# Kernel tuning notes

Measured on AMD Instinct MI355X. Metric: run time of the kernel, lower is better.

## Reference

```python
import jax, jax.numpy as jnp
import numpy as np
from jax import lax

B, N = 16, 2048
S0, S1, K = 256, 128, 32
EPS = 1e-5


def bn_relu(x, gamma, beta, axes):
    # training-mode BatchNorm (batch statistics) + ReLU; channel is last dim
    mean = jnp.mean(x, axis=axes, keepdims=True)
    var = jnp.var(x, axis=axes, keepdims=True)
    return jax.nn.relu((x - mean) * lax.rsqrt(var + EPS) * gamma + beta)


def fps(coords, s):
    # farthest point sampling, deterministic start at index 0. coords [B,N,3]
    b, n, _ = coords.shape
    def body(carry, _):
        dist, far = carry
        centroid = jnp.take_along_axis(coords, far[:, None, None], axis=1)  # [B,1,3]
        d = jnp.sum((coords - centroid) ** 2, axis=-1)                      # [B,N]
        dist = jnp.minimum(dist, d)
        return (dist, jnp.argmax(dist, axis=-1).astype(jnp.int32)), far
    init = (jnp.full((b, n), 1e10, coords.dtype), jnp.zeros((b,), jnp.int32))
    _, idx = lax.scan(body, init, None, length=s)
    return jnp.transpose(idx)  # [B,s]


def gather_points(pts, idx):
    # pts [B,N,C], idx [B,...] int -> [B,...,C]
    flat = idx.reshape(idx.shape[0], -1)[..., None]  # [B,M,1]
    out = jnp.take_along_axis(pts, flat, axis=1)     # [B,M,C]
    return out.reshape(*idx.shape, pts.shape[-1])


def sample_and_knn_group(s, k, coords, features):
    # coords [B,N,3], features [B,N,C] -> new_xyz [B,s,3], agg [B,s,k,2C]
    fps_idx = fps(coords, s)
    new_xyz = gather_points(coords, fps_idx)      # [B,s,3]
    center = gather_points(features, fps_idx)     # [B,s,C]
    d2 = jnp.sum((new_xyz[:, :, None, :] - coords[:, None, :, :]) ** 2, axis=-1)  # [B,s,N]
    _, knn_idx = lax.top_k(-d2, k)                # k smallest distances
    grouped = gather_points(features, knn_idx)    # [B,s,k,C]
    agg = jnp.concatenate(
        [grouped - center[:, :, None, :],
         jnp.broadcast_to(center[:, :, None, :], grouped.shape)], axis=-1)
    return new_xyz, agg


def sg_block(coords, features, s, k, w, gamma, beta):
    # conv1x1 -> BN -> ReLU -> max over k neighbors
    new_xyz, nf = sample_and_knn_group(s, k, coords, features)  # nf [B,s,k,d]
    h = jnp.einsum('bskd,od->bsko', nf, w)
    h = bn_relu(h, gamma, beta, axes=(0, 1, 2))
    return new_xyz, jnp.max(h, axis=2)  # [B,s,out]


def setup_inputs() -> dict:
    key = jax.random.key(0)
    ks = jax.random.split(key, 5)
    return {
        'x': jax.random.normal(ks[0], (B, 3, N), jnp.float32),
        'w1': jax.random.normal(ks[1], (64, 3), jnp.float32) * (1.0 / np.sqrt(3)),
        'g1': jnp.ones((64,), jnp.float32), 'b1': jnp.zeros((64,), jnp.float32),
        'w2': jax.random.normal(ks[2], (64, 64), jnp.float32) * 0.125,
        'g2': jnp.ones((64,), jnp.float32), 'b2': jnp.zeros((64,), jnp.float32),
        'w_sg0': jax.random.normal(ks[3], (128, 128), jnp.float32) * (1.0 / np.sqrt(128)),
        'g_sg0': jnp.ones((128,), jnp.float32), 'b_sg0': jnp.zeros((128,), jnp.float32),
        'w_sg1': jax.random.normal(ks[4], (256, 256), jnp.float32) * (1.0 / np.sqrt(256)),
        'g_sg1': jnp.ones((256,), jnp.float32), 'b_sg1': jnp.zeros((256,), jnp.float32),
    }


def reference(x, w1, g1, b1, w2, g2, b2, w_sg0, g_sg0, b_sg0, w_sg1, g_sg1, b_sg1):
    coords = jnp.transpose(x, (0, 2, 1))                   # [B,N,3]
    f = bn_relu(jnp.einsum('bnc,oc->bno', coords, w1), g1, b1, axes=(0, 1))  # [B,N,64]
    f = bn_relu(jnp.einsum('bnc,oc->bno', f, w2), g2, b2, axes=(0, 1))       # [B,N,64]
    xyz1, f1 = sg_block(coords, f, S0, K, w_sg0, g_sg0, b_sg0)   # [B,S0,128]
    _, f2 = sg_block(xyz1, f1, S1, K, w_sg1, g_sg1, b_sg1)       # [B,S1,256]
    return jnp.transpose(f2, (0, 2, 1))                           # [B,256,S1]
```

## Files before the change

### kernel.cpp

```cpp
#include <hip/hip_runtime.h>
#include <float.h>

#define BATCH 16
#define NPTS  2048
#define NS0   256
#define NS1   128
#define KK    32
#define EPSV  1e-5f
#define MROWS 32768.0f
#define M0F   131072.0f
#define M1F   65536.0f

__device__ __forceinline__ float sqdist(float ax,float ay,float az,float bx,float by,float bz){
  float dx=__fsub_rn(ax,bx), dy=__fsub_rn(ay,by), dz=__fsub_rn(az,bz);
  return __fadd_rn(__fadd_rn(__fmul_rn(dx,dx),__fmul_rn(dy,dy)),__fmul_rn(dz,dz));
}

template<int CTRL,int RM>
__device__ __forceinline__ float dpp_fmax_s(float x){
  int t = __builtin_amdgcn_update_dpp((int)0xFF800000, __float_as_int(x), CTRL, RM, 0xf, false);
  return fmaxf(x, __int_as_float(t));
}
template<int CTRL,int RM>
__device__ __forceinline__ float dpp_fmin_s(float x){
  int t = __builtin_amdgcn_update_dpp(0x7F800000, __float_as_int(x), CTRL, RM, 0xf, false);
  return fminf(x, __int_as_float(t));
}
template<int CTRL,int RM>
__device__ __forceinline__ unsigned dpp_umin_s(unsigned x){
  unsigned t = (unsigned)__builtin_amdgcn_update_dpp(-1, (int)x, CTRL, RM, 0xf, false);
  return t<x ? t : x;
}
__device__ __forceinline__ void wave_argmax_f32(float v, unsigned idx, float& mall, int& sel){
  float m=v;
  m=dpp_fmax_s<0x111,0xf>(m); m=dpp_fmax_s<0x112,0xf>(m); m=dpp_fmax_s<0x114,0xf>(m);
  m=dpp_fmax_s<0x118,0xf>(m); m=dpp_fmax_s<0x142,0xa>(m); m=dpp_fmax_s<0x143,0xc>(m);
  mall = __int_as_float(__builtin_amdgcn_readlane(__float_as_int(m),63));
  unsigned c = (v==mall)? idx : 0xFFFFFFFFu;
  c=dpp_umin_s<0x111,0xf>(c); c=dpp_umin_s<0x112,0xf>(c); c=dpp_umin_s<0x114,0xf>(c);
  c=dpp_umin_s<0x118,0xf>(c); c=dpp_umin_s<0x142,0xa>(c); c=dpp_umin_s<0x143,0xc>(c);
  sel = (int)(unsigned)__builtin_amdgcn_readlane((int)c,63);
}
__device__ __forceinline__ int wave_argmin_f32(float v, unsigned idx){
  float m=v;
  m=dpp_fmin_s<0x111,0xf>(m); m=dpp_fmin_s<0x112,0xf>(m); m=dpp_fmin_s<0x114,0xf>(m);
  m=dpp_fmin_s<0x118,0xf>(m); m=dpp_fmin_s<0x142,0xa>(m); m=dpp_fmin_s<0x143,0xc>(m);
  float mall = __int_as_float(__builtin_amdgcn_readlane(__float_as_int(m),63));
  unsigned c = (v==mall)? idx : 0xFFFFFFFFu;
  c=dpp_umin_s<0x111,0xf>(c); c=dpp_umin_s<0x112,0xf>(c); c=dpp_umin_s<0x114,0xf>(c);
  c=dpp_umin_s<0x118,0xf>(c); c=dpp_umin_s<0x142,0xa>(c); c=dpp_umin_s<0x143,0xc>(c);
  return (int)(unsigned)__builtin_amdgcn_readlane((int)c,63);
}


__device__ void embed1_body(int bid, const float* __restrict__ x, const float* __restrict__ w1,
                            float* __restrict__ coords, float* __restrict__ t1){
  __shared__ float w[192];
  __shared__ float xs[3][64];
  __shared__ float fin[64][65];
  int tid = threadIdx.x;
  if (tid < 192) w[tid] = w1[tid];
  int base = bid*64;
  int b = base / NPTS, n0 = base % NPTS;
  if (tid < 192){
    int ch = tid>>6, i = tid&63;
    xs[ch][i] = x[((size_t)b*3+ch)*NPTS + n0 + i];
  }
  __syncthreads();
  if (tid < 64){
    coords[(size_t)(base+tid)*3+0]=xs[0][tid];
    coords[(size_t)(base+tid)*3+1]=xs[1][tid];
    coords[(size_t)(base+tid)*3+2]=xs[2][tid];
  }
  int p = tid>>2, c0 = (tid&3)<<4;
  float cx=xs[0][p], cy=xs[1][p], cz=xs[2][p];
  #pragma unroll
  for(int j=0;j<16;j++){
    int c = c0+j;
    fin[p][c] = cx*w[c*3+0] + cy*w[c*3+1] + cz*w[c*3+2];
  }
  __syncthreads();
  for(int i=tid;i<4096;i+=256){
    int pp=i>>6, c=i&63;
    t1[(size_t)base*64 + i] = fin[pp][c];
  }
}

__device__ void wt_body(int gid, const float* __restrict__ w0, float* __restrict__ wt0,
                        const float* __restrict__ w1, float* __restrict__ wt1){
  if(gid < 128*128){
    int o = gid % 128, c = gid / 128;
    wt0[gid] = w0[o*128 + c];
  } else {
    int g2 = gid - 128*128;
    if(g2 >= 256*256) return;
    int o = g2 % 256, c = g2 / 256;
    wt1[g2] = w1[o*256 + c];
  }
}

__device__ void statsA_body(int blk, const float* __restrict__ t,
                            float* __restrict__ accS, float* __restrict__ accQ){
  int c = threadIdx.x;
  int r0 = blk*128;
  float s=0.f, q=0.f;
  for(int r=0;r<128;r++){
    float v = t[(size_t)(r0+r)*64 + c];
    s+=v; q+=v*v;
  }
  atomicAdd(accS+c, s);
  atomicAdd(accQ+c, q);
}

__device__ void embed2_body(int bid, const float* __restrict__ t1, const float* __restrict__ w2,
                            const float* __restrict__ accS, const float* __restrict__ accQ,
                            const float* __restrict__ g1, const float* __restrict__ b1,
                            float* __restrict__ t2,
                            float* __restrict__ acc2S, float* __restrict__ acc2Q,
                            float* ls, float* lq, char* smem){
  float (*fin)[64] = (float(*)[64])smem;
  float* sm = (float*)smem + 4096;
  float* sr = sm+64; float* sg = sr+64; float* sb = sg+64;
  int tid = threadIdx.x;
  if (tid<64){
    float S=accS[tid], Q=accQ[tid];
    float m = S/MROWS, v = Q/MROWS - m*m; if(v<0.f) v=0.f;
    sm[tid]=m; sr[tid]=rsqrtf(v+EPSV); sg[tid]=g1[tid]; sb[tid]=b1[tid];
    ls[tid]=0.f; lq[tid]=0.f;
  }
  __syncthreads();
  int base = bid*64;
  for(int i=tid;i<4096;i+=256){
    int p=i>>6, c=i&63;
    float v = t1[(size_t)(base+p)*64 + c];
    v = (v - sm[c])*sr[c]*sg[c] + sb[c];
    fin[p][c] = v>0.f ? v : 0.f;
  }
  __syncthreads();
  int o = tid & 63, p0 = tid>>6;
  float acc[16];
  #pragma unroll
  for(int i=0;i<16;i++) acc[i]=0.f;
  for(int cc=0; cc<64; cc+=4){
    float4 wv = *(const float4*)(w2 + o*64 + cc);
    #pragma unroll
    for(int i=0;i<16;i++){
      float4 f4 = *(const float4*)&fin[p0 + i*4][cc];
      acc[i] += f4.x*wv.x + f4.y*wv.y + f4.z*wv.z + f4.w*wv.w;
    }
  }
  float s=0.f,q=0.f;
  #pragma unroll
  for(int i=0;i<16;i++){
    float v = acc[i];
    t2[(size_t)(base+p0+i*4)*64 + o] = v;
    s+=v; q+=v*v;
  }
  atomicAdd(&ls[o], s);
  atomicAdd(&lq[o], q);
  __syncthreads();
  if(tid<64){ atomicAdd(acc2S+tid, ls[tid]); atomicAdd(acc2Q+tid, lq[tid]); }
}

template<int P, int S, int T>
__device__ void fps_body(int b, const float* __restrict__ x, int* __restrict__ outIdx,
                         float* __restrict__ outXyz, char* smem){
  constexpr int PPT = P/T;
  constexpr int NW  = T/64;
  float* sx=(float*)smem; float* sy=sx+P; float* sz=sy+P;
  int* sidx=(int*)(sz+P);
  unsigned long long* rv64=(unsigned long long*)(sidx+S);
  int tid = threadIdx.x;
  const float* xb = x + (size_t)b*3*P;
  float px[PPT], py[PPT], pz[PPT], dist[PPT];
  #pragma unroll
  for(int i=0;i<PPT;i++){
    int n = i*T + tid;
    float X=xb[n], Y=xb[P+n], Z=xb[2*P+n];
    px[i]=X; py[i]=Y; pz[i]=Z; dist[i]=1e10f;
    sx[n]=X; sy[n]=Y; sz[n]=Z;
  }
  __syncthreads();
  int cur = 0;
  float cx=sx[0], cy=sy[0], cz=sz[0];
  for(int s=0;s<S;s++){
    if(tid==0) sidx[s]=cur;
    if(s==S-1) break;
    float bv=-FLT_MAX; int bi=0;
    #pragma unroll
    for(int i=0;i<PPT;i++){
      float d = sqdist(px[i],py[i],pz[i],cx,cy,cz);
      float nd = fminf(dist[i], d);
      dist[i]=nd;
      int n = i*T + tid;
      if(nd>bv){ bv=nd; bi=n; }
    }
    float mall; int sel;
    wave_argmax_f32(bv,(unsigned)bi,mall,sel);
    int sl = s & 1;
    if((tid&63)==0) rv64[sl*NW+(tid>>6)] = ((unsigned long long)__float_as_uint(mall)<<32)|(unsigned)(~sel);
    __syncthreads();
    unsigned long long wk = rv64[sl*NW];
    #pragma unroll
    for(int w=1;w<NW;w++){ unsigned long long t = rv64[sl*NW+w]; if(t>wk) wk=t; }
    cur = (int)(~(unsigned)wk);
    cx=sx[cur]; cy=sy[cur]; cz=sz[cur];
  }
  __syncthreads();
  for(int i=tid; i<S; i+=T){
    int id = sidx[i];
    outIdx[b*S+i] = id;
    outXyz[((size_t)b*S+i)*3+0] = sx[id];
    outXyz[((size_t)b*S+i)*3+1] = sy[id];
    outXyz[((size_t)b*S+i)*3+2] = sz[id];
  }
}

template<int P, int S>
__device__ void fps_wave_body(int b, const float* __restrict__ pts, int* __restrict__ outIdx,
                              float* __restrict__ outXyz, char* smem){
  constexpr int PPT = P/64;
  float4* sp = (float4*)smem;
  int* sidx = (int*)(smem + P*sizeof(float4));
  int lane = threadIdx.x;
  const float* p = pts + (size_t)b*P*3;
  float px[PPT], py[PPT], pz[PPT], dist[PPT];
  #pragma unroll
  for(int i=0;i<PPT;i++){
    int n = i*64 + lane;
    float X=p[n*3], Y=p[n*3+1], Z=p[n*3+2];
    px[i]=X; py[i]=Y; pz[i]=Z; dist[i]=1e10f;
    sp[n] = make_float4(X,Y,Z,0.f);
  }
  __syncthreads();
  int cur = 0;
  float cx=sp[0].x, cy=sp[0].y, cz=sp[0].z;
  for(int s=0;s<S;s++){
    if(lane==0) sidx[s]=cur;
    if(s==S-1) break;
    float bv=-FLT_MAX; int bi=0;
    #pragma unroll
    for(int i=0;i<PPT;i++){
      float d = sqdist(px[i],py[i],pz[i],cx,cy,cz);
      float nd = fminf(dist[i], d);
      dist[i]=nd;
      int n = i*64 + lane;
      if(nd>bv){ bv=nd; bi=n; }
    }
    float mall; int sel;
    wave_argmax_f32(bv,(unsigned)bi,mall,sel);
    cur = sel;
    float4 cp = sp[cur];
    cx=cp.x; cy=cp.y; cz=cp.z;
  }
  __syncthreads();
  for(int i=lane; i<S; i+=64){
    int id = sidx[i];
    float4 cp = sp[id];
    outIdx[b*S+i] = id;
    outXyz[((size_t)b*S+i)*3+0] = cp.x;
    outXyz[((size_t)b*S+i)*3+1] = cp.y;
    outXyz[((size_t)b*S+i)*3+2] = cp.z;
  }
}

template<int P>
__device__ void knn_body(int bq, const float* __restrict__ pts, const float* __restrict__ q,
                         int S, int* __restrict__ knn){
  constexpr int E = P/64;
  int lane = threadIdx.x;
  int b = bq / S;
  const float* p = pts + (size_t)b*P*3;
  float qx=q[(size_t)bq*3], qy=q[(size_t)bq*3+1], qz=q[(size_t)bq*3+2];
  float dl[E];
  float b1=FLT_MAX, b2=FLT_MAX;
  unsigned i1=0xFFFFFFFFu, i2=0xFFFFFFFFu, consumed=0u;
  #pragma unroll
  for(int i=0;i<E;i++){
    unsigned n = i*64 + lane;
    float v = sqdist(qx,qy,qz,p[n*3],p[n*3+1],p[n*3+2]);
    dl[i] = v;
    bool lt1 = v<b1, lt2 = v<b2;
    float    nb2 = lt1 ? b1 : (lt2 ? v : b2);
    unsigned ni2 = lt1 ? i1 : (lt2 ? n : i2);
    b1 = lt1 ? v : b1; i1 = lt1 ? n : i1;
    b2 = nb2; i2 = ni2;
  }
  for(int j=0;j<KK;j++){
    int sel = wave_argmin_f32(b1, i1);
    if(lane==0) knn[(size_t)bq*KK+j] = sel;
    if((sel & 63) == lane){
      consumed |= 1u << (sel >> 6);
      b1 = b2; i1 = i2;
      b2 = FLT_MAX; i2 = 0xFFFFFFFFu;
      if(b1 == FLT_MAX){
        #pragma unroll
        for(int i=0;i<E;i++){
          float v = ((consumed>>i)&1u) ? FLT_MAX : dl[i];
          unsigned n = i*64 + lane;
          bool lt1 = v<b1, lt2 = v<b2;
          float    nb2 = lt1 ? b1 : (lt2 ? v : b2);
          unsigned ni2 = lt1 ? i1 : (lt2 ? n : i2);
          b1 = lt1 ? v : b1; i1 = lt1 ? n : i1;
          b2 = nb2; i2 = ni2;
        }
      }
    }
  }
}

template<int C, int P, int MODE>
__device__ void pass1_body(int bq, const float* __restrict__ feats, const float* __restrict__ feats2,
                           const int* __restrict__ knn,
                           const int* __restrict__ fpsIdx, const float* __restrict__ WT,
                           float* __restrict__ hmax, float* __restrict__ hmin,
                           float* __restrict__ part, int S,
                           const float* __restrict__ accS, const float* __restrict__ accQ,
                           const float* __restrict__ bg, const float* __restrict__ bb){
  constexpr int O   = 2*C;
  constexpr int TPB = C;
  constexpr int C4  = C/4;
  constexpr int OG  = O/8;
  constexpr int LDC = C+4;
  __shared__ __align__(16) float gfp[KK*LDC];
  __shared__ __align__(16) float cf[C];
  __shared__ __align__(16) float sa[C], sbb[C];
  __shared__ float sct[O];
  int tid = threadIdx.x;
  int b = bq / S;
  const float* fb = feats + (size_t)b*P*C;
  const float* fb2 = (MODE==2) ? feats2 + (size_t)b*P*C : nullptr;
  int ci = fpsIdx[bq];
  {
    float Mv = (MODE==1) ? MROWS : M0F;
    float S_=accS[tid], Q_=accQ[tid];
    float m = S_/Mv, vv = Q_/Mv - m*m; if(vv<0.f) vv=0.f;
    float a = rsqrtf(vv+EPSV)*bg[tid];
    float sh = bb[tid] - m*a;
    sa[tid]=a; sbb[tid]=sh;
    float raw;
    if(MODE==1) raw = fb[(size_t)ci*C + tid];
    else        raw = (a>=0.f) ? fb[(size_t)ci*C + tid] : fb2[(size_t)ci*C + tid];
    float cv = a*raw + sh;
    cf[tid] = cv>0.f ? cv : 0.f;
  }
  __syncthreads();
  for(int i=tid; i<KK*C4; i+=TPB){
    int k = i/C4, d4 = i - k*C4;
    size_t row = (size_t)knn[(size_t)bq*KK+k]*C;
    float4 a4 = *(const float4*)&sa[d4*4];
    float4 s4 = *(const float4*)&sbb[d4*4];
    float4 c4 = *(const float4*)&cf[d4*4];
    float4 g  = ((const float4*)(fb + row))[d4];
    float4 r;
    if(MODE==2){
      float4 g2 = ((const float4*)(fb2 + row))[d4];
      float gx = (a4.x>=0.f? g.x : g2.x)*a4.x + s4.x; gx = gx>0.f?gx:0.f;
      float gy = (a4.y>=0.f? g.y : g2.y)*a4.y + s4.y; gy = gy>0.f?gy:0.f;
      float gz = (a4.z>=0.f? g.z : g2.z)*a4.z + s4.z; gz = gz>0.f?gz:0.f;
      float gw = (a4.w>=0.f? g.w : g2.w)*a4.w + s4.w; gw = gw>0.f?gw:0.f;
      r.x=gx-c4.x; r.y=gy-c4.y; r.z=gz-c4.z; r.w=gw-c4.w;
    } else {
      float gx = a4.x*g.x+s4.x; gx = gx>0.f?gx:0.f;
      float gy = a4.y*g.y+s4.y; gy = gy>0.f?gy:0.f;
      float gz = a4.z*g.z+s4.z; gz = gz>0.f?gz:0.f;
      float gw = a4.w*g.w+s4.w; gw = gw>0.f?gw:0.f;
      r.x=gx-c4.x; r.y=gy-c4.y; r.z=gz-c4.z; r.w=gw-c4.w;
    }
    *(float4*)&gfp[k*LDC + d4*4] = r;
  }
  __syncthreads();
  {
    int o2 = tid*2;
    float ct0=0.f, ct1=0.f;
    for(int c=0;c<C;c+=4){
      float4 c4 = *(const float4*)&cf[c];
      #pragma unroll
      for(int t=0;t<4;t++){
        float cv = ((const float*)&c4)[t];
        float2 wh = *(const float2*)&WT[(size_t)(C+c+t)*O + o2];
        ct0 += cv*wh.x; ct1 += cv*wh.y;
      }
    }
    sct[o2]=ct0; sct[o2+1]=ct1;
  }
  __syncthreads();
  int kg = tid / OG;
  int og = tid % OG;
  float acc[8][8];
  #pragma unroll
  for(int a=0;a<8;a++)
    #pragma unroll
    for(int bb2=0;bb2<8;bb2++) acc[a][bb2]=0.f;
  for(int dc=0; dc<C4; dc++){
    float4 g4[8];
    #pragma unroll
    for(int jk=0;jk<8;jk++) g4[jk] = *(const float4*)&gfp[(kg*8+jk)*LDC + dc*4];
    #pragma unroll
    for(int t=0;t<4;t++){
      const float* wrow = WT + (size_t)(dc*4+t)*O + og*8;
      float4 wa = *(const float4*)wrow;
      float4 wb = *(const float4*)(wrow+4);
      #pragma unroll
      for(int jk=0;jk<8;jk++){
        float gs = ((const float*)&g4[jk])[t];
        acc[jk][0] += gs*wa.x; acc[jk][1] += gs*wa.y; acc[jk][2] += gs*wa.z; acc[jk][3] += gs*wa.w;
        acc[jk][4] += gs*wb.x; acc[jk][5] += gs*wb.y; acc[jk][6] += gs*wb.z; acc[jk][7] += gs*wb.w;
      }
    }
  }
  float tmx[8],tmn[8],tsm[8],tsq[8];
  #pragma unroll
  for(int jo=0;jo<8;jo++){
    int o = og*8+jo;
    float ct = sct[o];
    float s=0.f,q=0.f,mx=-FLT_MAX,mn=FLT_MAX;
    #pragma unroll
    for(int jk=0;jk<8;jk++){
      float h = acc[jk][jo] + ct;
      s+=h; q+=h*h; mx=fmaxf(mx,h); mn=fminf(mn,h);
    }
    tmx[jo]=mx; tmn[jo]=mn; tsm[jo]=s; tsq[jo]=q;
  }
  if constexpr (TPB==64){
    #pragma unroll
    for(int jo=0;jo<8;jo++){
      tmx[jo]=fmaxf(tmx[jo],__shfl_xor(tmx[jo],16)); tmx[jo]=fmaxf(tmx[jo],__shfl_xor(tmx[jo],32));
      tmn[jo]=fminf(tmn[jo],__shfl_xor(tmn[jo],16)); tmn[jo]=fminf(tmn[jo],__shfl_xor(tmn[jo],32));
      tsm[jo]+=__shfl_xor(tsm[jo],16); tsm[jo]+=__shfl_xor(tsm[jo],32);
      tsq[jo]+=__shfl_xor(tsq[jo],16); tsq[jo]+=__shfl_xor(tsq[jo],32);
    }
    if(tid<OG){
      #pragma unroll
      for(int jo=0;jo<8;jo++){
        int o = tid*8+jo;
        hmax[(size_t)bq*O+o]=tmx[jo]; hmin[(size_t)bq*O+o]=tmn[jo];
        part[(size_t)bq*2*O+o]=tsm[jo]; part[(size_t)bq*2*O+O+o]=tsq[jo];
      }
    }
  } else {
    #pragma unroll
    for(int jo=0;jo<8;jo++){
      tmx[jo]=fmaxf(tmx[jo],__shfl_xor(tmx[jo],32));
      tmn[jo]=fminf(tmn[jo],__shfl_xor(tmn[jo],32));
      tsm[jo]+=__shfl_xor(tsm[jo],32);
      tsq[jo]+=__shfl_xor(tsq[jo],32);
    }
    int wv = tid>>6;
    if((tid&63)<32){
      int og_ = tid&31;
      size_t rb = (size_t)bq*2 + wv;
      #pragma unroll
      for(int jo=0;jo<8;jo++){
        int o = og_*8+jo;
        hmax[rb*O+o]=tmx[jo]; hmin[rb*O+o]=tmn[jo];
        part[rb*2*O+o]=tsm[jo]; part[rb*2*O+O+o]=tsq[jo];
      }
    }
  }
}


__global__ __launch_bounds__(256) void k_embed1_wt(const float* __restrict__ x, const float* __restrict__ w1,
                         float* __restrict__ coords, float* __restrict__ t1,
                         const float* __restrict__ wsg0, float* __restrict__ wt0,
                         const float* __restrict__ wsg1, float* __restrict__ wt1,
                         float* __restrict__ accz){
  if(blockIdx.x < 512) embed1_body(blockIdx.x, x, w1, coords, t1);
  else if(blockIdx.x < 832) wt_body((blockIdx.x-512)*256 + threadIdx.x, wsg0, wt0, wsg1, wt1);
  else {
    int tid = threadIdx.x;
    accz[tid]=0.f; accz[tid+256]=0.f; accz[tid+512]=0.f; accz[tid+768]=0.f;
  }
}

__global__ __launch_bounds__(64) void k_statsA(const float* __restrict__ t,
                         float* __restrict__ accS, float* __restrict__ accQ){
  statsA_body(blockIdx.x, t, accS, accQ);
}

__global__ __launch_bounds__(256, 1) void k_fps0_embed2(const float* __restrict__ x,
                         int* __restrict__ fps0, float* __restrict__ xyz0,
                         const float* __restrict__ t1, const float* __restrict__ w2,
                         const float* __restrict__ acc1S, const float* __restrict__ acc1Q,
                         const float* __restrict__ g1, const float* __restrict__ b1,
                         float* __restrict__ t2,
                         float* __restrict__ acc2S, float* __restrict__ acc2Q){
  extern __shared__ char smem[];
  __shared__ float ls[64], lq[64];
  if(blockIdx.x < BATCH) fps_body<NPTS,NS0,256>(blockIdx.x, x, fps0, xyz0, smem);
  else embed2_body(blockIdx.x-BATCH, t1, w2, acc1S, acc1Q, g1, b1, t2, acc2S, acc2Q, ls, lq, smem);
}

__global__ __launch_bounds__(64, 4) void k_fps1_knn0(const float* __restrict__ xyz0,
                         int* __restrict__ fps1, float* __restrict__ xyz1,
                         const float* __restrict__ coords, int* __restrict__ knn0){
  extern __shared__ char smem[];
  if(blockIdx.x < BATCH) fps_wave_body<NS0,NS1>(blockIdx.x, xyz0, fps1, xyz1, smem);
  else knn_body<NPTS>(blockIdx.x-BATCH, coords, xyz0, NS0, knn0);
}

__global__ __launch_bounds__(64, 2) void k_pass1a_knn1(const float* __restrict__ t2,
                         const int* __restrict__ knn0, const int* __restrict__ fps0,
                         const float* __restrict__ wt0,
                         float* __restrict__ hmax0, float* __restrict__ hmin0, float* __restrict__ part0,
                         const float* __restrict__ acc2S, const float* __restrict__ acc2Q,
                         const float* __restrict__ g2, const float* __restrict__ b2,
                         const float* __restrict__ xyz0, const float* __restrict__ xyz1,
                         int* __restrict__ knn1){
  if(blockIdx.x < BATCH*NS0)
    pass1_body<64,NPTS,1>(blockIdx.x, t2, nullptr, knn0, fps0, wt0, hmax0, hmin0, part0, NS0,
                          acc2S, acc2Q, g2, b2);
  else
    knn_body<NS0>(blockIdx.x-BATCH*NS0, xyz0, xyz1, NS1, knn1);
}

__global__ __launch_bounds__(128, 2) void k_pass1b(const float* __restrict__ hmax0,
                         const float* __restrict__ hmin0,
                         const int* __restrict__ knn1, const int* __restrict__ fps1,
                         const float* __restrict__ wt1,
                         float* __restrict__ hmax1, float* __restrict__ hmin1, float* __restrict__ part1,
                         const float* __restrict__ accB0S, const float* __restrict__ accB0Q,
                         const float* __restrict__ gsg0, const float* __restrict__ bsg0){
  pass1_body<128,NS0,2>(blockIdx.x, hmax0, hmin0, knn1, fps1, wt1, hmax1, hmin1, part1, NS1,
                        accB0S, accB0Q, gsg0, bsg0);
}

__global__ __launch_bounds__(256) void k_statsB(const float* __restrict__ part, int W,
                                                float* __restrict__ acc){
  int tid = threadIdx.x;
  int r0 = blockIdx.x*64;
  for(int c=tid; c<W; c+=256){
    float a=0.f;
    for(int r=0;r<64;r++) a += part[(size_t)(r0+r)*W + c];
    atomicAdd(acc+c, a);
  }
}

__global__ __launch_bounds__(256) void k_post1tr(const float* __restrict__ hmax, const float* __restrict__ hmin,
        const float* __restrict__ aS, const float* __restrict__ aQ,
        const float* __restrict__ g, const float* __restrict__ bb, float* __restrict__ out){
  __shared__ float ssc[64], ssh[64];
  __shared__ float tile[64][129];
  int tid = threadIdx.x;
  int blk = blockIdx.x; int b = blk>>2; int c0 = (blk&3)*64;
  if(tid<64){
    int o = c0+tid;
    float m = aS[o]/M1F, v = aQ[o]/M1F - m*m; if(v<0.f) v=0.f;
    float sc = rsqrtf(v+EPSV)*g[o];
    ssc[tid]=sc; ssh[tid]=bb[o]-m*sc;
  }
  __syncthreads();
  for(int i=tid; i<128*64; i+=256){
    int r=i>>6, ch=i&63;
    size_t rb = (size_t)(b*NS1+r)*2;
    float sc = ssc[ch];
    float va = hmax[rb*256 + c0+ch], vb = hmax[(rb+1)*256 + c0+ch];
    float wa = hmin[rb*256 + c0+ch], wb = hmin[(rb+1)*256 + c0+ch];
    float h = (sc>=0.f) ? fmaxf(va,vb) : fminf(wa,wb);
    float v = h*sc + ssh[ch];
    tile[ch][r] = v>0.f ? v : 0.f;
  }
  __syncthreads();
  for(int i=tid; i<64*128; i+=256){
    int ch=i>>7, s=i&127;
    out[(size_t)b*(256*NS1) + (size_t)(c0+ch)*NS1 + s] = tile[ch][s];
  }
}

extern "C" void kernel_launch(void* const* d_in, const int* in_sizes, int n_in,
                              void* d_out, int out_size, void* d_ws, size_t ws_size,
                              hipStream_t stream){
  const float* x    = (const float*)d_in[0];
  const float* w1   = (const float*)d_in[1];
  const float* g1   = (const float*)d_in[2];
  const float* b1   = (const float*)d_in[3];
  const float* w2   = (const float*)d_in[4];
  const float* g2   = (const float*)d_in[5];
  const float* b2   = (const float*)d_in[6];
  const float* wsg0 = (const float*)d_in[7];
  const float* gsg0 = (const float*)d_in[8];
  const float* bsg0 = (const float*)d_in[9];
  const float* wsg1 = (const float*)d_in[10];
  const float* gsg1 = (const float*)d_in[11];
  const float* bsg1 = (const float*)d_in[12];
  float* out = (float*)d_out;

  float* wsf = (float*)d_ws;
  float* coords = wsf;                    wsf += BATCH*NPTS*3;
  float* t1     = wsf;                    wsf += BATCH*NPTS*64;
  float* t2     = wsf;                    wsf += BATCH*NPTS*64;
  float* acc1S=wsf; wsf+=64;  float* acc1Q=wsf; wsf+=64;
  float* acc2S=wsf; wsf+=64;  float* acc2Q=wsf; wsf+=64;
  float* accB0=wsf; wsf+=256;
  float* accB1=wsf; wsf+=512;
  int*   fps0 = (int*)wsf;                wsf += BATCH*NS0;
  float* xyz0 = wsf;                      wsf += BATCH*NS0*3;
  int*   knn0 = (int*)wsf;                wsf += BATCH*NS0*KK;
  float* hmax0= wsf;                      wsf += BATCH*NS0*128;
  float* hmin0= wsf;                      wsf += BATCH*NS0*128;
  float* part0= wsf;                      wsf += BATCH*NS0*2*128;
  int*   fps1 = (int*)wsf;                wsf += BATCH*NS1;
  float* xyz1 = wsf;                      wsf += BATCH*NS1*3;
  int*   knn1 = (int*)wsf;                wsf += BATCH*NS1*KK;
  float* wt0  = wsf;                      wsf += 128*128;
  float* wt1  = wsf;                      wsf += 256*256;
  float* part1 = t1;
  float* hmax1 = t2;
  float* hmin1 = t2 + BATCH*NS1*2*256;

  const int DYN_L3 = (NPTS*3 + NS0)*4 + 2*4*8;
  const int DYN_L4 = NS0*16 + NS1*4;

  k_embed1_wt<<<dim3(833), dim3(256), 0, stream>>>(x, w1, coords, t1, wsg0, wt0, wsg1, wt1, acc1S);
  k_statsA<<<dim3(256), dim3(64), 0, stream>>>(t1, acc1S, acc1Q);
  k_fps0_embed2<<<dim3(BATCH+512), dim3(256), DYN_L3, stream>>>(x, fps0, xyz0,
                                                  t1, w2, acc1S, acc1Q, g1, b1, t2, acc2S, acc2Q);
  k_fps1_knn0<<<dim3(BATCH + BATCH*NS0), dim3(64), DYN_L4, stream>>>(xyz0, fps1, xyz1, coords, knn0);
  k_pass1a_knn1<<<dim3(BATCH*NS0 + BATCH*NS1), dim3(64), 0, stream>>>(t2, knn0, fps0, wt0,
                                                  hmax0, hmin0, part0,
                                                  acc2S, acc2Q, g2, b2,
                                                  xyz0, xyz1, knn1);
  k_statsB<<<dim3(64), dim3(256), 0, stream>>>(part0, 256, accB0);
  k_pass1b<<<dim3(BATCH*NS1), dim3(128), 0, stream>>>(hmax0, hmin0, knn1, fps1, wt1,
                                                  hmax1, hmin1, part1,
                                                  accB0, accB0+128, gsg0, bsg0);
  k_statsB<<<dim3(64), dim3(256), 0, stream>>>(part1, 512, accB1);
  k_post1tr<<<dim3(64), dim3(256), 0, stream>>>(hmax1, hmin1, accB1, accB1+256, gsg1, bsg1, out);
}
```

Baseline: 402.4 us.

## Fuse KNN selection into pass1 kernels via shared-memory neighbor lists

```diff
diff --git a/kernel.cpp b/kernel.cpp
--- a/kernel.cpp
+++ b/kernel.cpp
@@ -265,13 +265,10 @@
 }
 
 template<int P>
-__device__ void knn_body(int bq, const float* __restrict__ pts, const float* __restrict__ q,
-                         int S, int* __restrict__ knn){
+__device__ void knn_compute(const float* __restrict__ p, float qx, float qy, float qz,
+                            int* outRow){
   constexpr int E = P/64;
-  int lane = threadIdx.x;
-  int b = bq / S;
-  const float* p = pts + (size_t)b*P*3;
-  float qx=q[(size_t)bq*3], qy=q[(size_t)bq*3+1], qz=q[(size_t)bq*3+2];
+  int lane = threadIdx.x & 63;
   float dl[E];
   float b1=FLT_MAX, b2=FLT_MAX;
   unsigned i1=0xFFFFFFFFu, i2=0xFFFFFFFFu, consumed=0u;
@@ -288,7 +285,7 @@
   }
   for(int j=0;j<KK;j++){
     int sel = wave_argmin_f32(b1, i1);
-    if(lane==0) knn[(size_t)bq*KK+j] = sel;
+    if(lane==0) outRow[j] = sel;
     if((sel & 63) == lane){
       consumed |= 1u << (sel >> 6);
       b1 = b2; i1 = i2;
@@ -311,26 +308,26 @@
 
 template<int C, int P, int MODE>
 __device__ void pass1_body(int bq, const float* __restrict__ feats, const float* __restrict__ feats2,
-                           const int* __restrict__ knn,
-                           const int* __restrict__ fpsIdx, const float* __restrict__ WT,
+                           const int* knnrow, int ci, const float* __restrict__ WT,
                            float* __restrict__ hmax, float* __restrict__ hmin,
                            float* __restrict__ part, int S,
                            const float* __restrict__ accS, const float* __restrict__ accQ,
-                           const float* __restrict__ bg, const float* __restrict__ bb){
+                           const float* __restrict__ bg, const float* __restrict__ bb,
+                           char* smem){
   constexpr int O   = 2*C;
   constexpr int TPB = C;
   constexpr int C4  = C/4;
   constexpr int OG  = O/8;
   constexpr int LDC = C+4;
-  __shared__ __align__(16) float gfp[KK*LDC];
-  __shared__ __align__(16) float cf[C];
-  __shared__ __align__(16) float sa[C], sbb[C];
-  __shared__ float sct[O];
+  float* gfp = (float*)smem;
+  float* cf  = gfp + KK*LDC;
+  float* sa  = cf + C;
+  float* sbb = sa + C;
+  float* sct = sbb + C;
   int tid = threadIdx.x;
   int b = bq / S;
   const float* fb = feats + (size_t)b*P*C;
   const float* fb2 = (MODE==2) ? feats2 + (size_t)b*P*C : nullptr;
-  int ci = fpsIdx[bq];
   {
     float Mv = (MODE==1) ? MROWS : M0F;
     float S_=accS[tid], Q_=accQ[tid];
@@ -347,7 +344,7 @@
   __syncthreads();
   for(int i=tid; i<KK*C4; i+=TPB){
     int k = i/C4, d4 = i - k*C4;
-    size_t row = (size_t)knn[(size_t)bq*KK+k]*C;
+    size_t row = (size_t)knnrow[k]*C;
     float4 a4 = *(const float4*)&sa[d4*4];
     float4 s4 = *(const float4*)&sbb[d4*4];
     float4 c4 = *(const float4*)&cf[d4*4];
@@ -492,38 +489,27 @@
   else embed2_body(blockIdx.x-BATCH, t1, w2, acc1S, acc1Q, g1, b1, t2, acc2S, acc2Q, ls, lq, smem);
 }
 
-__global__ __launch_bounds__(64, 4) void k_fps1_knn0(const float* __restrict__ xyz0,
+__global__ __launch_bounds__(64, 2) void k_fps1_p1a(const float* __restrict__ xyz0,
                          int* __restrict__ fps1, float* __restrict__ xyz1,
-                         const float* __restrict__ coords, int* __restrict__ knn0){
-  extern __shared__ char smem[];
-  if(blockIdx.x < BATCH) fps_wave_body<NS0,NS1>(blockIdx.x, xyz0, fps1, xyz1, smem);
-  else knn_body<NPTS>(blockIdx.x-BATCH, coords, xyz0, NS0, knn0);
-}
-
-__global__ __launch_bounds__(64, 2) void k_pass1a_knn1(const float* __restrict__ t2,
-                         const int* __restrict__ knn0, const int* __restrict__ fps0,
-                         const float* __restrict__ wt0,
+                         const float* __restrict__ coords, const float* __restrict__ t2,
+                         const int* __restrict__ fps0, const float* __restrict__ wt0,
                          float* __restrict__ hmax0, float* __restrict__ hmin0, float* __restrict__ part0,
                          const float* __restrict__ acc2S, const float* __restrict__ acc2Q,
-                         const float* __restrict__ g2, const float* __restrict__ b2,
-                         const float* __restrict__ xyz0, const float* __restrict__ xyz1,
-                         int* __restrict__ knn1){
-  if(blockIdx.x < BATCH*NS0)
-    pass1_body<64,NPTS,1>(blockIdx.x, t2, nullptr, knn0, fps0, wt0, hmax0, hmin0, part0, NS0,
-                          acc2S, acc2Q, g2, b2);
-  else
-    knn_body<NS0>(blockIdx.x-BATCH*NS0, xyz0, xyz1, NS1, knn1);
-}
-
-__global__ __launch_bounds__(128, 2) void k_pass1b(const float* __restrict__ hmax0,
-                         const float* __restrict__ hmin0,
-                         const int* __restrict__ knn1, const int* __restrict__ fps1,
-                         const float* __restrict__ wt1,
-                         float* __restrict__ hmax1, float* __restrict__ hmin1, float* __restrict__ part1,
-                         const float* __restrict__ accB0S, const float* __restrict__ accB0Q,
-                         const float* __restrict__ gsg0, const float* __restrict__ bsg0){
-  pass1_body<128,NS0,2>(blockIdx.x, hmax0, hmin0, knn1, fps1, wt1, hmax1, hmin1, part1, NS1,
-                        accB0S, accB0Q, gsg0, bsg0);
+                         const float* __restrict__ g2, const float* __restrict__ b2){
+  __shared__ __align__(16) char SU[10112];
+  if(blockIdx.x < BATCH){
+    fps_wave_body<NS0,NS1>(blockIdx.x, xyz0, fps1, xyz1, SU);
+    return;
+  }
+  int bq = blockIdx.x - BATCH;
+  int b = bq / NS0;
+  int* sknn = (int*)(SU + 9984);
+  const float* pc = coords + (size_t)b*NPTS*3;
+  float qx=xyz0[(size_t)bq*3], qy=xyz0[(size_t)bq*3+1], qz=xyz0[(size_t)bq*3+2];
+  knn_compute<NPTS>(pc, qx, qy, qz, sknn);
+  __syncthreads();
+  pass1_body<64,NPTS,1>(bq, t2, nullptr, sknn, fps0[bq], wt0, hmax0, hmin0, part0, NS0,
+                        acc2S, acc2Q, g2, b2, SU);
 }
 
 __global__ __launch_bounds__(256) void k_statsB(const float* __restrict__ part, int W,
@@ -535,6 +521,27 @@
     for(int r=0;r<64;r++) a += part[(size_t)(r0+r)*W + c];
     atomicAdd(acc+c, a);
   }
+}
+
+__global__ __launch_bounds__(128, 2) void k_knn1_p1b(const float* __restrict__ xyz0,
+                         const float* __restrict__ xyz1, const int* __restrict__ fps1,
+                         const float* __restrict__ hmax0, const float* __restrict__ hmin0,
+                         const float* __restrict__ wt1,
+                         float* __restrict__ hmax1, float* __restrict__ hmin1, float* __restrict__ part1,
+                         const float* __restrict__ accB0S, const float* __restrict__ accB0Q,
+                         const float* __restrict__ gsg0, const float* __restrict__ bsg0){
+  __shared__ __align__(16) char SU[19584];
+  int bq = blockIdx.x;
+  int b = bq / NS1;
+  int* sknn = (int*)(SU + 19456);
+  if(threadIdx.x < 64){
+    const float* pts = xyz0 + (size_t)b*NS0*3;
+    float qx=xyz1[(size_t)bq*3], qy=xyz1[(size_t)bq*3+1], qz=xyz1[(size_t)bq*3+2];
+    knn_compute<NS0>(pts, qx, qy, qz, sknn);
+  }
+  __syncthreads();
+  pass1_body<128,NS0,2>(bq, hmax0, hmin0, sknn, fps1[bq], wt1, hmax1, hmin1, part1, NS1,
+                        accB0S, accB0Q, gsg0, bsg0, SU);
 }
 
 __global__ __launch_bounds__(256) void k_post1tr(const float* __restrict__ hmax, const float* __restrict__ hmin,
@@ -596,13 +603,11 @@
   float* accB1=wsf; wsf+=512;
   int*   fps0 = (int*)wsf;                wsf += BATCH*NS0;
   float* xyz0 = wsf;                      wsf += BATCH*NS0*3;
-  int*   knn0 = (int*)wsf;                wsf += BATCH*NS0*KK;
   float* hmax0= wsf;                      wsf += BATCH*NS0*128;
   float* hmin0= wsf;                      wsf += BATCH*NS0*128;
   float* part0= wsf;                      wsf += BATCH*NS0*2*128;
   int*   fps1 = (int*)wsf;                wsf += BATCH*NS1;
   float* xyz1 = wsf;                      wsf += BATCH*NS1*3;
-  int*   knn1 = (int*)wsf;                wsf += BATCH*NS1*KK;
   float* wt0  = wsf;                      wsf += 128*128;
   float* wt1  = wsf;                      wsf += 256*256;
   float* part1 = t1;
@@ -610,19 +615,18 @@
   float* hmin1 = t2 + BATCH*NS1*2*256;
 
   const int DYN_L3 = (NPTS*3 + NS0)*4 + 2*4*8;
-  const int DYN_L4 = NS0*16 + NS1*4;
 
   k_embed1_wt<<<dim3(833), dim3(256), 0, stream>>>(x, w1, coords, t1, wsg0, wt0, wsg1, wt1, acc1S);
   k_statsA<<<dim3(256), dim3(64), 0, stream>>>(t1, acc1S, acc1Q);
   k_fps0_embed2<<<dim3(BATCH+512), dim3(256), DYN_L3, stream>>>(x, fps0, xyz0,
                                                   t1, w2, acc1S, acc1Q, g1, b1, t2, acc2S, acc2Q);
-  k_fps1_knn0<<<dim3(BATCH + BATCH*NS0), dim3(64), DYN_L4, stream>>>(xyz0, fps1, xyz1, coords, knn0);
-  k_pass1a_knn1<<<dim3(BATCH*NS0 + BATCH*NS1), dim3(64), 0, stream>>>(t2, knn0, fps0, wt0,
+  k_fps1_p1a<<<dim3(BATCH + BATCH*NS0), dim3(64), 0, stream>>>(xyz0, fps1, xyz1,
+                                                  coords, t2, fps0, wt0,
                                                   hmax0, hmin0, part0,
-                                                  acc2S, acc2Q, g2, b2,
-                                                  xyz0, xyz1, knn1);
+                                                  acc2S, acc2Q, g2, b2);
   k_statsB<<<dim3(64), dim3(256), 0, stream>>>(part0, 256, accB0);
-  k_pass1b<<<dim3(BATCH*NS1), dim3(128), 0, stream>>>(hmax0, hmin0, knn1, fps1, wt1,
+  k_knn1_p1b<<<dim3(BATCH*NS1), dim3(128), 0, stream>>>(xyz0, xyz1, fps1,
+                                                  hmax0, hmin0, wt1,
                                                   hmax1, hmin1, part1,
                                                   accB0, accB0+128, gsg0, bsg0);
   k_statsB<<<dim3(64), dim3(256), 0, stream>>>(part1, 512, accB1);
```

New measurement: 388.4 us. 1.04x faster.
